# Kernel tuning notes

Hardware: AMD Instinct MI355X
Metric: run time of the kernel (lower is better)

## Reference

```python
import jax, jax.numpy as jnp
import numpy as np

B, T, N, E = 128, 24, 300, 9000
H, O = 1, 4            # num_heads, out_feats
GRU_H = 12
NUM_AIRPORTS, HORIZON = 300, 4


def setup_inputs() -> dict:
    key = jax.random.key(0)
    ks = jax.random.split(key, 16)
    inp = {
        "x": jax.random.normal(ks[0], (B, T, N, 1), jnp.float32),
        "ew": jax.random.uniform(ks[1], (B, T, E, 1), jnp.float32),
        "src": jax.random.randint(ks[2], (E,), 0, N, jnp.int32),
        "dst": jax.random.randint(ks[3], (E,), 0, N, jnp.int32),
        # EdgeGATConv params (fc / fc_edge have no bias in DGL GAT-style convs)
        "w_node": jax.random.normal(ks[4], (H * O, 1), jnp.float32) * 0.5,
        "w_edge": jax.random.normal(ks[5], (H * O, 1), jnp.float32) * 0.5,
        "attn_l": jax.random.normal(ks[6], (H, O), jnp.float32) * 0.5,
        "attn_r": jax.random.normal(ks[7], (H, O), jnp.float32) * 0.5,
        "attn_e": jax.random.normal(ks[8], (H, O), jnp.float32) * 0.5,
        "gat_bias": jnp.zeros((H * O,), jnp.float32),
        # GRU (single layer, input 4 -> hidden 12); gates stacked [r|z|n]
        "w_ih": jax.random.normal(ks[9], (3 * GRU_H, H * O), jnp.float32) * 0.3,
        "w_hh": jax.random.normal(ks[10], (3 * GRU_H, GRU_H), jnp.float32) * 0.3,
        "b_ih": jnp.zeros((3 * GRU_H,), jnp.float32),
        "b_hh": jnp.zeros((3 * GRU_H,), jnp.float32),
        # fc: gru_out -> num_airports * horizon
        "fc_w": jax.random.normal(ks[11], (NUM_AIRPORTS * HORIZON, GRU_H), jnp.float32) * 0.1,
        "fc_b": jnp.zeros((NUM_AIRPORTS * HORIZON,), jnp.float32),
    }
    return inp


def _edge_gat_pool(x, ew, src, dst, w_node, w_edge, attn_l, attn_r, attn_e, gat_bias):
    """Batched DGL EdgeGATConv over G=B*T graphs (shared topology) + mean pool."""
    b, t = x.shape[0], x.shape[1]
    G = b * t
    xf = x.reshape(G, N, 1)
    ef = ew.reshape(G, E, 1)
    # node / edge projections -> [G, *, H, O]
    ft = jnp.einsum('gni,fi->gnf', xf, w_node).reshape(G, N, H, O)
    fe = jnp.einsum('gei,fi->gef', ef, w_edge).reshape(G, E, H, O)
    el = jnp.einsum('gnho,ho->gnh', ft, attn_l)          # [G,N,H]
    er = jnp.einsum('gnho,ho->gnh', ft, attn_r)          # [G,N,H]
    ee = jnp.einsum('geho,ho->geh', fe, attn_e)          # [G,E,H]
    e = jax.nn.leaky_relu(el[:, src] + er[:, dst] + ee, negative_slope=0.2)
    # edge softmax over incoming edges of each dst node
    m = jnp.full((G, N, H), -jnp.inf, e.dtype).at[:, dst].max(e)
    ex = jnp.exp(e - m[:, dst])                           # [G,E,H]
    den = jnp.zeros((G, N, H), e.dtype).at[:, dst].add(ex)
    a = ex / den[:, dst]
    # aggregate messages: sum_j alpha_ij * W h_j
    msg = ft[:, src] * a[..., None]                       # [G,E,H,O]
    rst = jnp.zeros((G, N, H, O), e.dtype).at[:, dst].add(msg)
    rst = rst + gat_bias.reshape(H, O)
    # flatten heads, mean-pool over nodes -> [B,T,H*O]
    return rst.reshape(G, N, H * O).mean(axis=1).reshape(b, t, H * O)


def _gru_last(seq, w_ih, w_hh, b_ih, b_hh):
    """torch nn.GRU (1 layer, batch_first), returns final hidden state [B,GRU_H]."""
    def cell(h, xt):
        gi = xt @ w_ih.T + b_ih
        gh = h @ w_hh.T + b_hh
        i_r, i_z, i_n = jnp.split(gi, 3, axis=-1)
        h_r, h_z, h_n = jnp.split(gh, 3, axis=-1)
        r = jax.nn.sigmoid(i_r + h_r)
        z = jax.nn.sigmoid(i_z + h_z)
        n = jnp.tanh(i_n + r * h_n)
        h_new = (1.0 - z) * n + z * h
        return h_new, None
    h0 = jnp.zeros((seq.shape[0], GRU_H), seq.dtype)
    hT, _ = jax.lax.scan(cell, h0, jnp.swapaxes(seq, 0, 1))
    return hT


def reference(x, ew, src, dst, w_node, w_edge, attn_l, attn_r, attn_e,
              gat_bias, w_ih, w_hh, b_ih, b_hh, fc_w, fc_b):
    pooled = _edge_gat_pool(x, ew, src, dst, w_node, w_edge,
                            attn_l, attn_r, attn_e, gat_bias)  # [B,T,4]
    # dropout(0.1) is identity in eval mode
    h_n = _gru_last(pooled, w_ih, w_hh, b_ih, b_hh)            # [B,12]
    return h_n @ fc_w.T + fc_b                                  # [B,1200]
```

## Files before the change

### kernel.cpp

```cpp
#include <hip/hip_runtime.h>
#include <math.h>

#define B_    128
#define T_    24
#define NN    300
#define EE    9000
#define GG    (B_ * T_)
#define GRUH  12
#define OUTF  1200

__global__ __launch_bounds__(1024) void build_csr(
    const int* __restrict__ src, const int* __restrict__ dst,
    int* __restrict__ row_ptr, int* __restrict__ csr_src, int* __restrict__ csr_pos)
{
    __shared__ int hist[16][512];
    __shared__ int cnt[512];
    __shared__ int bufA[512], bufB[512];
    const int tid  = threadIdx.x;
    const int wave = tid >> 6;

    for (int i = tid; i < 16 * 512; i += 1024) ((int*)hist)[i] = 0;
    __syncthreads();

    for (int e = tid; e < EE; e += 1024) atomicAdd(&hist[wave][dst[e]], 1);
    __syncthreads();

    if (tid < 512) {
        int s = 0;
#pragma unroll
        for (int w = 0; w < 16; w++) { int t = hist[w][tid]; hist[w][tid] = s; s += t; }
        cnt[tid] = s;
    }
    __syncthreads();

    int* cur = bufA; int* nxt = bufB;
    if (tid < 512) cur[tid] = cnt[tid];
    __syncthreads();
    for (int d = 1; d < 512; d <<= 1) {
        if (tid < 512) nxt[tid] = cur[tid] + (tid >= d ? cur[tid - d] : 0);
        __syncthreads();
        int* t = cur; cur = nxt; nxt = t;
    }
    if (tid <= NN) row_ptr[tid] = (tid == 0) ? 0 : cur[tid - 1];
    __syncthreads();

    if (tid < 512) {
        const int base = (tid == 0) ? 0 : cur[tid - 1];
#pragma unroll
        for (int w = 0; w < 16; w++) hist[w][tid] += base;
    }
    __syncthreads();

    for (int e = tid; e < EE; e += 1024) {
        const int d = dst[e];
        const int pos = atomicAdd(&hist[wave][d], 1);
        csr_src[pos] = src[e];
        csr_pos[e]   = pos;
    }
}

__global__ __launch_bounds__(512) void gat_pool(
    const float* __restrict__ x, const float* __restrict__ ew,
    const int* __restrict__ src, const int* __restrict__ dst,
    const float* __restrict__ w_node, const float* __restrict__ w_edge,
    const float* __restrict__ attn_l, const float* __restrict__ attn_r,
    const float* __restrict__ attn_e,
    const int* __restrict__ row_ptr, const int* __restrict__ csr_src,
    const int* __restrict__ csr_pos,
    float* __restrict__ S)
{
    __shared__ float xs[NN];
    __shared__ float evals[EE];
    __shared__ float red[8];

    const int g = blockIdx.x;
    const int tid = threadIdx.x;

    float cL = 0.f, cR = 0.f, cE = 0.f;
#pragma unroll
    for (int o = 0; o < 4; o++) {
        float wn = w_node[o];
        cL += wn * attn_l[o];
        cR += wn * attn_r[o];
        cE += w_edge[o] * attn_e[o];
    }

    const float* xrow = x + (size_t)g * NN;
    const float* erow = ew + (size_t)g * EE;

    for (int i = tid; i < NN; i += 512) xs[i] = xrow[i];
    __syncthreads();

    const float4* __restrict__ erow4 = (const float4*)erow;
    const int4*   __restrict__ src4  = (const int4*)src;
    const int4*   __restrict__ dst4  = (const int4*)dst;
    const int4*   __restrict__ pos4  = (const int4*)csr_pos;

#define PROC(sj, dj, pj, ev)                                        \
    {                                                               \
        float v = fmaf(cL, xs[(sj)], fmaf(cR, xs[(dj)], cE * (ev))); \
        v = (v >= 0.f) ? v : 0.2f * v;                              \
        evals[(pj)] = __expf(v);                                    \
    }

    for (int q = tid; q < EE / 4; q += 512) {
        const float4 e4 = erow4[q];
        const int4   s4 = src4[q];
        const int4   d4 = dst4[q];
        const int4   p4 = pos4[q];
        PROC(s4.x, d4.x, p4.x, e4.x);
        PROC(s4.y, d4.y, p4.y, e4.y);
        PROC(s4.z, d4.z, p4.z, e4.z);
        PROC(s4.w, d4.w, p4.w, e4.w);
    }
#undef PROC
    __syncthreads();

    float acc = 0.f;
    if (tid < NN) {
        const int beg = row_ptr[tid];
        const int end = row_ptr[tid + 1];
        float den = 0.f, num = 0.f;
        int i = beg;
        for (; i + 4 <= end; i += 4) {
            const float e0 = evals[i],     e1 = evals[i + 1];
            const float e2 = evals[i + 2], e3 = evals[i + 3];
            const int   s0 = csr_src[i],     s1 = csr_src[i + 1];
            const int   s2 = csr_src[i + 2], s3 = csr_src[i + 3];
            const float x0 = xs[s0], x1 = xs[s1], x2 = xs[s2], x3 = xs[s3];
            den += (e0 + e1) + (e2 + e3);
            num = fmaf(e0, x0, num); num = fmaf(e1, x1, num);
            num = fmaf(e2, x2, num); num = fmaf(e3, x3, num);
        }
        for (; i < end; i++) {
            const float e0 = evals[i];
            den += e0;
            num = fmaf(e0, xs[csr_src[i]], num);
        }
        if (end > beg) acc = num / den;
    }

    for (int off = 32; off > 0; off >>= 1) acc += __shfl_down(acc, off);
    if ((tid & 63) == 0) red[tid >> 6] = acc;
    __syncthreads();
    if (tid == 0) {
        float s = 0.f;
#pragma unroll
        for (int w = 0; w < 8; w++) s += red[w];
        S[g] = s;
    }
}

__device__ __forceinline__ float sigmoidf_(float v) { return 1.0f / (1.0f + __expf(-v)); }

__global__ __launch_bounds__(256) void gru_fc(
    const float* __restrict__ S,
    const float* __restrict__ w_node, const float* __restrict__ gat_bias,
    const float* __restrict__ w_ih, const float* __restrict__ w_hh,
    const float* __restrict__ b_ih, const float* __restrict__ b_hh,
    const float* __restrict__ fc_w, const float* __restrict__ fc_b,
    float* __restrict__ out)
{
    __shared__ float hsh[GRUH];
    const int b = blockIdx.x;
    const int tid = threadIdx.x;

    if (tid < 64) {
        float wn[4], gb[4];
#pragma unroll
        for (int i = 0; i < 4; i++) {
            wn[i] = w_node[i] * (1.0f / (float)NN);
            gb[i] = gat_bias[i];
        }
        float wih[4] = {0.f, 0.f, 0.f, 0.f};
        float whh[12];
#pragma unroll
        for (int j = 0; j < 12; j++) whh[j] = 0.f;
        float bih = 0.f, bhh = 0.f;
        if (tid < 36) {
#pragma unroll
            for (int i = 0; i < 4; i++)  wih[i] = w_ih[tid * 4 + i];
#pragma unroll
            for (int j = 0; j < 12; j++) whh[j] = w_hh[tid * 12 + j];
            bih = b_ih[tid];
            bhh = b_hh[tid];
        }
        float srow = (tid < T_) ? S[(size_t)b * T_ + tid] : 0.f;
        float hreg = 0.f;
        const int l = tid % 12;
        for (int t = 0; t < T_; t++) {
            float Sg = __shfl(srow, t);
            float gi = bih, gh = bhh;
#pragma unroll
            for (int i = 0; i < 4; i++) gi += (Sg * wn[i] + gb[i]) * wih[i];
#pragma unroll
            for (int j = 0; j < 12; j++) gh += __shfl(hreg, j) * whh[j];
            float a   = gi + gh;
            float aiz = __shfl(a, 12 + l);
            float gin = __shfl(gi, 24 + l);
            float ghn = __shfl(gh, 24 + l);
            if (tid < 12) {
                float r = sigmoidf_(a);
                float z = sigmoidf_(aiz);
                float n = tanhf(gin + r * ghn);
                hreg = (1.f - z) * n + z * hreg;
            }
        }
        if (tid < GRUH) hsh[tid] = hreg;
    }
    __syncthreads();

    float h0 = hsh[0], h1 = hsh[1], h2 = hsh[2],  h3 = hsh[3];
    float h4 = hsh[4], h5 = hsh[5], h6 = hsh[6],  h7 = hsh[7];
    float h8 = hsh[8], h9 = hsh[9], hA = hsh[10], hB = hsh[11];
    for (int j = tid; j < OUTF; j += 256) {
        const float4* w4 = (const float4*)(fc_w + (size_t)j * GRUH);
        const float4 a = w4[0], c = w4[1], d = w4[2];
        float o = fc_b[j];
        o += h0 * a.x + h1 * a.y + h2 * a.z + h3 * a.w;
        o += h4 * c.x + h5 * c.y + h6 * c.z + h7 * c.w;
        o += h8 * d.x + h9 * d.y + hA * d.z + hB * d.w;
        out[(size_t)b * OUTF + j] = o;
    }
}

extern "C" void kernel_launch(void* const* d_in, const int* in_sizes, int n_in,
                              void* d_out, int out_size, void* d_ws, size_t ws_size,
                              hipStream_t stream)
{
    const float* x        = (const float*)d_in[0];
    const float* ew       = (const float*)d_in[1];
    const int*   src      = (const int*)d_in[2];
    const int*   dst      = (const int*)d_in[3];
    const float* w_node   = (const float*)d_in[4];
    const float* w_edge   = (const float*)d_in[5];
    const float* attn_l   = (const float*)d_in[6];
    const float* attn_r   = (const float*)d_in[7];
    const float* attn_e   = (const float*)d_in[8];
    const float* gat_bias = (const float*)d_in[9];
    const float* w_ih     = (const float*)d_in[10];
    const float* w_hh     = (const float*)d_in[11];
    const float* b_ih     = (const float*)d_in[12];
    const float* b_hh     = (const float*)d_in[13];
    const float* fc_w     = (const float*)d_in[14];
    const float* fc_b     = (const float*)d_in[15];
    float* out = (float*)d_out;

    char* ws = (char*)d_ws;
    float* S       = (float*)ws;
    int*   row_ptr = (int*)(ws + GG * 4);
    int*   csr_src = row_ptr + 304;
    int*   csr_pos = csr_src + EE;

    build_csr<<<1, 1024, 0, stream>>>(src, dst, row_ptr, csr_src, csr_pos);
    gat_pool<<<GG, 512, 0, stream>>>(x, ew, src, dst, w_node, w_edge,
                                     attn_l, attn_r, attn_e,
                                     row_ptr, csr_src, csr_pos, S);
    gru_fc<<<B_, 256, 0, stream>>>(S, w_node, gat_bias, w_ih, w_hh,
                                   b_ih, b_hh, fc_w, fc_b, out);
}
```

Before: 254.8 us.

## Pack edge exp and weighted source value as half2, drop csr_src gather

The edge pass now stores each edge's exponentiated score and that score times the source feature together as one packed fp16 pair in shared memory. The aggregation pass then only reads and sums these pairs, so it no longer needs the csr_src index lookup or the indirect xs gather. The CSR build also orders destination segments by in-degree, so neighbouring threads get similar amounts of work and waves diverge less. In exchange, fp16 storage reduces accuracy, and the logit is clamped at 11 to avoid fp16 overflow, which changes results for any edge whose score exceeds that.

After: 227.4 us. 10.7% less time.

```diff
diff --git a/kernel.cpp b/kernel.cpp
--- a/kernel.cpp
+++ b/kernel.cpp
@@ -1,4 +1,5 @@
 #include <hip/hip_runtime.h>
+#include <hip/hip_fp16.h>
 #include <math.h>
 
 #define B_    128
@@ -11,13 +12,15 @@
 
 __global__ __launch_bounds__(1024) void build_csr(
     const int* __restrict__ src, const int* __restrict__ dst,
-    int* __restrict__ row_ptr, int* __restrict__ csr_src, int* __restrict__ csr_pos)
+    int* __restrict__ row_ptr, int* __restrict__ csr_pos)
 {
     __shared__ int hist[16][512];
     __shared__ int cnt[512];
+    __shared__ int rankv[512];
     __shared__ int bufA[512], bufB[512];
     const int tid  = threadIdx.x;
     const int wave = tid >> 6;
+    (void)src;
 
     for (int i = tid; i < 16 * 512; i += 1024) ((int*)hist)[i] = 0;
     __syncthreads();
@@ -33,19 +36,31 @@
     }
     __syncthreads();
 
+    if (tid < NN) {
+        const int d = cnt[tid];
+        int r = 0;
+        for (int m = 0; m < NN; m++) {
+            const int dm = cnt[m];
+            r += (dm > d) || (dm == d && m < tid);
+        }
+        rankv[tid] = r;
+    }
+    if (tid < 512) bufA[tid] = 0;
+    __syncthreads();
+    if (tid < NN) bufA[rankv[tid]] = cnt[tid];
+    __syncthreads();
+
     int* cur = bufA; int* nxt = bufB;
-    if (tid < 512) cur[tid] = cnt[tid];
-    __syncthreads();
     for (int d = 1; d < 512; d <<= 1) {
         if (tid < 512) nxt[tid] = cur[tid] + (tid >= d ? cur[tid - d] : 0);
         __syncthreads();
         int* t = cur; cur = nxt; nxt = t;
     }
     if (tid <= NN) row_ptr[tid] = (tid == 0) ? 0 : cur[tid - 1];
-    __syncthreads();
 
     if (tid < 512) {
-        const int base = (tid == 0) ? 0 : cur[tid - 1];
+        int base = 0;
+        if (tid < NN) { const int r = rankv[tid]; base = (r == 0) ? 0 : cur[r - 1]; }
 #pragma unroll
         for (int w = 0; w < 16; w++) hist[w][tid] += base;
     }
@@ -54,8 +69,7 @@
     for (int e = tid; e < EE; e += 1024) {
         const int d = dst[e];
         const int pos = atomicAdd(&hist[wave][d], 1);
-        csr_src[pos] = src[e];
-        csr_pos[e]   = pos;
+        csr_pos[e] = pos;
     }
 }
 
@@ -65,12 +79,11 @@
     const float* __restrict__ w_node, const float* __restrict__ w_edge,
     const float* __restrict__ attn_l, const float* __restrict__ attn_r,
     const float* __restrict__ attn_e,
-    const int* __restrict__ row_ptr, const int* __restrict__ csr_src,
-    const int* __restrict__ csr_pos,
+    const int* __restrict__ row_ptr, const int* __restrict__ csr_pos,
     float* __restrict__ S)
 {
     __shared__ float xs[NN];
-    __shared__ float evals[EE];
+    __shared__ __align__(16) unsigned int evals[EE];
     __shared__ float red[8];
 
     const int g = blockIdx.x;
@@ -96,11 +109,17 @@
     const int4*   __restrict__ dst4  = (const int4*)dst;
     const int4*   __restrict__ pos4  = (const int4*)csr_pos;
 
-#define PROC(sj, dj, pj, ev)                                        \
-    {                                                               \
-        float v = fmaf(cL, xs[(sj)], fmaf(cR, xs[(dj)], cE * (ev))); \
-        v = (v >= 0.f) ? v : 0.2f * v;                              \
-        evals[(pj)] = __expf(v);                                    \
+#define PROC(sj, dj, pj, ev)                                         \
+    {                                                                \
+        const float xsv = xs[(sj)];                                  \
+        float v = fmaf(cL, xsv, fmaf(cR, xs[(dj)], cE * (ev)));      \
+        v = (v >= 0.f) ? v : 0.2f * v;                               \
+        v = fminf(v, 11.0f);                                         \
+        const float ex = __expf(v);                                  \
+        union { __half2 h2; unsigned int u; } c;                     \
+        c.h2 = __halves2half2(__float2half_rn(ex),                   \
+                              __float2half_rn(ex * xsv));            \
+        evals[(pj)] = c.u;                                           \
     }
 
     for (int q = tid; q < EE / 4; q += 512) {
@@ -122,20 +141,27 @@
         const int end = row_ptr[tid + 1];
         float den = 0.f, num = 0.f;
         int i = beg;
+        if ((i & 1) && i < end) {
+            union { unsigned int u; __half2 h2; } c; c.u = evals[i++];
+            const float2 f = __half22float2(c.h2);
+            den += f.x; num += f.y;
+        }
         for (; i + 4 <= end; i += 4) {
-            const float e0 = evals[i],     e1 = evals[i + 1];
-            const float e2 = evals[i + 2], e3 = evals[i + 3];
-            const int   s0 = csr_src[i],     s1 = csr_src[i + 1];
-            const int   s2 = csr_src[i + 2], s3 = csr_src[i + 3];
-            const float x0 = xs[s0], x1 = xs[s1], x2 = xs[s2], x3 = xs[s3];
-            den += (e0 + e1) + (e2 + e3);
-            num = fmaf(e0, x0, num); num = fmaf(e1, x1, num);
-            num = fmaf(e2, x2, num); num = fmaf(e3, x3, num);
+            const uint2 a = *(const uint2*)(evals + i);
+            const uint2 b = *(const uint2*)(evals + i + 2);
+            union { unsigned int u; __half2 h2; } c0, c1, c2, c3;
+            c0.u = a.x; c1.u = a.y; c2.u = b.x; c3.u = b.y;
+            const float2 f0 = __half22float2(c0.h2);
+            const float2 f1 = __half22float2(c1.h2);
+            const float2 f2 = __half22float2(c2.h2);
+            const float2 f3 = __half22float2(c3.h2);
+            den += (f0.x + f1.x) + (f2.x + f3.x);
+            num += (f0.y + f1.y) + (f2.y + f3.y);
         }
         for (; i < end; i++) {
-            const float e0 = evals[i];
-            den += e0;
-            num = fmaf(e0, xs[csr_src[i]], num);
+            union { unsigned int u; __half2 h2; } c; c.u = evals[i];
+            const float2 f = __half22float2(c.h2);
+            den += f.x; num += f.y;
         }
         if (end > beg) acc = num / den;
     }
@@ -249,13 +275,12 @@
     char* ws = (char*)d_ws;
     float* S       = (float*)ws;
     int*   row_ptr = (int*)(ws + GG * 4);
-    int*   csr_src = row_ptr + 304;
-    int*   csr_pos = csr_src + EE;
-
-    build_csr<<<1, 1024, 0, stream>>>(src, dst, row_ptr, csr_src, csr_pos);
+    int*   csr_pos = row_ptr + 304;
+
+    build_csr<<<1, 1024, 0, stream>>>(src, dst, row_ptr, csr_pos);
     gat_pool<<<GG, 512, 0, stream>>>(x, ew, src, dst, w_node, w_edge,
                                      attn_l, attn_r, attn_e,
-                                     row_ptr, csr_src, csr_pos, S);
+                                     row_ptr, csr_pos, S);
     gru_fc<<<B_, 256, 0, stream>>>(S, w_node, gat_bias, w_ih, w_hh,
                                    b_ih, b_hh, fc_w, fc_b, out);
 }
```
